# Performance work log

Measured on AMD Instinct MI355X. Metric: run time of the kernel, lower is better.

## Reference

```python
import jax, jax.numpy as jnp
import numpy as np

N = 50000      # total nodes
E = 500000     # edges
D = 128        # in_channels
B = 50         # graphs in batch
NPG = N // B   # nodes per graph (equal-sized graphs)
RATIO = 0.5
ALPHA = 0.6


def setup_inputs() -> dict:
    key = jax.random.key(0)
    ks = jax.random.split(key, 8)
    x = jax.random.normal(ks[0], (N, D), dtype=jnp.float32)
    edge_index = jax.random.randint(ks[1], (2, E), 0, N, dtype=jnp.int32)
    batch = jnp.repeat(jnp.arange(B, dtype=jnp.int32), NPG)  # sorted, equal blocks
    s = 1.0 / np.sqrt(D)
    # GCNConv(D,1) for structure score
    W_s = jax.random.normal(ks[2], (D, 1), dtype=jnp.float32) * s
    b_s = jnp.zeros((1,), dtype=jnp.float32)
    # Linear(D,1) for feature score
    W_f = jax.random.normal(ks[3], (1, D), dtype=jnp.float32) * s
    b_f = jnp.zeros((1,), dtype=jnp.float32)
    # GCNConv(D,D) fusion layer
    W_fu = jax.random.normal(ks[4], (D, D), dtype=jnp.float32) * s
    b_fu = jnp.zeros((D,), dtype=jnp.float32)
    return {"x": x, "edge_index": edge_index, "batch": batch,
            "W_s": W_s, "b_s": b_s, "W_f": W_f, "b_f": b_f,
            "W_fu": W_fu, "b_fu": b_fu}


def gcn_conv(x, src, dst, W, b, n):
    """PyG GCNConv: add self loops, symmetric D^-1/2 (A+I) D^-1/2 @ (xW) + b."""
    xw = x @ W                                  # [n, out]
    loop = jnp.arange(n, dtype=src.dtype)
    s = jnp.concatenate([src, loop])
    d = jnp.concatenate([dst, loop])
    deg = jax.ops.segment_sum(jnp.ones_like(s, dtype=xw.dtype), d, num_segments=n)
    dinv = jax.lax.rsqrt(jnp.maximum(deg, 1e-12))
    norm = dinv[s] * dinv[d]                    # [E+n]
    out = jax.ops.segment_sum(norm[:, None] * xw[s], d, num_segments=n)
    return out + b


def reference(x, edge_index, batch, W_s, b_s, W_f, b_f, W_fu, b_fu):
    src, dst = edge_index[0], edge_index[1]
    # fused score: alpha * structure (GCN) + (1-alpha) * feature (Linear)
    score_s = gcn_conv(x, src, dst, W_s, b_s, N)[:, 0]          # [N]
    score_f = (x @ W_f.T + b_f)[:, 0]                           # [N]
    score = jnp.tanh(ALPHA * score_s + (1.0 - ALPHA) * score_f)
    # per-graph top-k (equal-sized graphs -> dense [B, NPG] view, like the torch topk)
    k = int(np.ceil(RATIO * NPG))
    dense = score.reshape(B, NPG)
    order = jnp.argsort(-dense, axis=-1)                        # descending
    offsets = (jnp.arange(B, dtype=jnp.int32) * NPG)[:, None]
    perm = (order[:, :k].astype(jnp.int32) + offsets).reshape(-1)  # [B*k]
    # fusion conv on full graph, then gather selected nodes
    x_fused = gcn_conv(x, src, dst, W_fu, b_fu, N)              # [N, D]
    x_ae = x_fused[perm]                                        # [B*k, D]
    x_out = x_ae * score[perm][:, None]                         # multiplier == 1
    batch_out = batch[perm]
    # filter_adj: remap node ids, keep edges with both endpoints selected
    nodemap = jnp.full((N,), -1, dtype=jnp.int32).at[perm].set(
        jnp.arange(perm.shape[0], dtype=jnp.int32))
    r, c = nodemap[src], nodemap[dst]
    m = (r >= 0) & (c >= 0)
    edge_index_new = jnp.stack([r[m], c[m]], axis=0)
    return (x_out, edge_index_new, batch_out, perm, x_ae)
```

## Files before the change

### kernel.cpp

```cpp
#include <hip/hip_runtime.h>
#include <math.h>

#define N_NODES 50000
#define N_EDGES 500000
#define DIM     128
#define NGRAPH  50
#define NPGC    1000
#define KSEL    500
#define SORT_N  1024
#define NBE     489
#define NBN     49
#define GEMM_BLKS 391
#define DEG_BLKS  1954
#define DOTS_BLKS 12500
#define NDINV     196
#define GATH_BLKS 6250


__global__ __launch_bounds__(256) void k1_gemm_deg(const float* __restrict__ x,
                                                   const float* __restrict__ W,
                                                   float* __restrict__ xw,
                                                   const int* __restrict__ dst,
                                                   int* __restrict__ deg) {
    __shared__ float lds[16384];
    int t = threadIdx.x;
    if (blockIdx.x >= GEMM_BLKS) {
        int e = (blockIdx.x - GEMM_BLKS) * 256 + t;
        if (e < N_EDGES) atomicAdd(&deg[dst[e]], 1);
        return;
    }
    float* Wt = lds;
    float* Xt = lds + 64 * DIM;
    int cg = t & 15;
    int ng = t >> 4;
    int node_base = blockIdx.x * 128;

    float4 acc[8][2];
    #pragma unroll
    for (int nn = 0; nn < 8; nn++) {
        acc[nn][0] = make_float4(0.f, 0.f, 0.f, 0.f);
        acc[nn][1] = make_float4(0.f, 0.f, 0.f, 0.f);
    }
    for (int half = 0; half < 2; half++) {
        const float4* Wg = (const float4*)(W + half * 64 * DIM);
        float4* Wl = (float4*)Wt;
        #pragma unroll
        for (int i = 0; i < 8; i++) {
            int f = t + i * 256;
            Wl[f] = Wg[f];
        }
        #pragma unroll
        for (int i = 0; i < 8; i++) {
            int f = t + i * 256;
            int row = f >> 4, col = f & 15;
            int node = node_base + row;
            float4 v = make_float4(0.f, 0.f, 0.f, 0.f);
            if (node < N_NODES) v = *(const float4*)&x[(size_t)node * DIM + half * 64 + col * 4];
            *(float4*)&Xt[(row << 6) + ((col ^ (row & 15)) << 2)] = v;
        }
        __syncthreads();
        #pragma unroll 2
        for (int kc = 0; kc < 16; kc++) {
            int k = kc << 2;
            float4 wa[4], wb[4];
            #pragma unroll
            for (int kk = 0; kk < 4; kk++) {
                wa[kk] = *(const float4*)&Wt[(k + kk) * DIM + (cg << 2)];
                wb[kk] = *(const float4*)&Wt[(k + kk) * DIM + (cg << 2) + 64];
            }
            int csw = (kc ^ ng) << 2;
            #pragma unroll
            for (int nn = 0; nn < 8; nn++) {
                float4 xv = *(const float4*)&Xt[((ng + (nn << 4)) << 6) + csw];
                acc[nn][0].x += xv.x * wa[0].x + xv.y * wa[1].x + xv.z * wa[2].x + xv.w * wa[3].x;
                acc[nn][0].y += xv.x * wa[0].y + xv.y * wa[1].y + xv.z * wa[2].y + xv.w * wa[3].y;
                acc[nn][0].z += xv.x * wa[0].z + xv.y * wa[1].z + xv.z * wa[2].z + xv.w * wa[3].z;
                acc[nn][0].w += xv.x * wa[0].w + xv.y * wa[1].w + xv.z * wa[2].w + xv.w * wa[3].w;
                acc[nn][1].x += xv.x * wb[0].x + xv.y * wb[1].x + xv.z * wb[2].x + xv.w * wb[3].x;
                acc[nn][1].y += xv.x * wb[0].y + xv.y * wb[1].y + xv.z * wb[2].y + xv.w * wb[3].y;
                acc[nn][1].z += xv.x * wb[0].z + xv.y * wb[1].z + xv.z * wb[2].z + xv.w * wb[3].z;
                acc[nn][1].w += xv.x * wb[0].w + xv.y * wb[1].w + xv.z * wb[2].w + xv.w * wb[3].w;
            }
        }
        __syncthreads();
    }
    #pragma unroll
    for (int nn = 0; nn < 8; nn++) {
        int node = node_base + ng + (nn << 4);
        if (node < N_NODES) {
            *(float4*)&xw[(size_t)node * DIM + (cg << 2)]      = acc[nn][0];
            *(float4*)&xw[(size_t)node * DIM + (cg << 2) + 64] = acc[nn][1];
        }
    }
}


__global__ __launch_bounds__(256) void k2_dots_scan_dinv(const int* __restrict__ deg,
                                                         int* __restrict__ rowoff,
                                                         int* __restrict__ bsumsN,
                                                         const float* __restrict__ x,
                                                         const float* __restrict__ Ws,
                                                         const float* __restrict__ Wf,
                                                         const float* __restrict__ bf,
                                                         double* __restrict__ pack,
                                                         float* __restrict__ dinvf,
                                                         double* __restrict__ sf) {
    int t = threadIdx.x;
    int lane = t & 63, wid = t >> 6;
    int bid = blockIdx.x;
    if (bid < DOTS_BLKS) {
        int node = bid * 4 + wid;
        const float* xr = x + (size_t)node * DIM;
        double x1 = (double)xr[lane], x2 = (double)xr[lane + 64];
        double ps = x1 * (double)Ws[lane] + x2 * (double)Ws[lane + 64];
        double pf = x1 * (double)Wf[lane] + x2 * (double)Wf[lane + 64];
        for (int off = 32; off > 0; off >>= 1) {
            ps += __shfl_down(ps, off, 64);
            pf += __shfl_down(pf, off, 64);
        }
        if (lane == 0) {
            pack[2 * node + 1] = ps;
            sf[node] = pf + (double)bf[0];
        }
        return;
    }
    if (bid < DOTS_BLKS + NBN) {
        __shared__ int ws4[4];
        int base = (bid - DOTS_BLKS) * 1024 + t * 4;
        int v0 = (base + 0 < N_NODES) ? deg[base + 0] : 0;
        int v1 = (base + 1 < N_NODES) ? deg[base + 1] : 0;
        int v2 = (base + 2 < N_NODES) ? deg[base + 2] : 0;
        int v3 = (base + 3 < N_NODES) ? deg[base + 3] : 0;
        int s4 = v0 + v1 + v2 + v3;
        int incl = s4;
        #pragma unroll
        for (int off = 1; off < 64; off <<= 1) {
            int u = __shfl_up(incl, off, 64);
            if (lane >= off) incl += u;
        }
        if (lane == 63) ws4[wid] = incl;
        __syncthreads();
        int woff = 0;
        #pragma unroll
        for (int w = 0; w < 4; w++) if (w < wid) woff += ws4[w];
        int excl = incl - s4 + woff;
        if (base + 0 < N_NODES) rowoff[base + 0] = excl;
        if (base + 1 < N_NODES) rowoff[base + 1] = excl + v0;
        if (base + 2 < N_NODES) rowoff[base + 2] = excl + v0 + v1;
        if (base + 3 < N_NODES) rowoff[base + 3] = excl + v0 + v1 + v2;
        if (t == 255) bsumsN[bid - DOTS_BLKS] = woff + incl;
        return;
    }
    int i = (bid - DOTS_BLKS - NBN) * 256 + t;
    if (i < N_NODES) {
        double di = 1.0 / sqrt((double)(deg[i] + 1));
        pack[2 * i] = di;
        dinvf[i] = (float)di;
    }
}


__global__ __launch_bounds__(256) void k3_csr(const int* __restrict__ src,
                                              const int* __restrict__ dst,
                                              const int* __restrict__ rowoff,
                                              const int* __restrict__ bsumsN,
                                              int* __restrict__ cursor,
                                              int* __restrict__ csr) {
    __shared__ int bsN[64];
    int t = threadIdx.x;
    if (t < 64) {
        int v = (t < NBN) ? bsumsN[t] : 0;
        int incl = v;
        #pragma unroll
        for (int off = 1; off < 64; off <<= 1) {
            int u = __shfl_up(incl, off, 64);
            if (t >= off) incl += u;
        }
        bsN[t] = incl - v;
    }
    __syncthreads();
    int e = blockIdx.x * 256 + t;
    if (e >= N_EDGES) return;
    int d = dst[e];
    int pos = rowoff[d] + bsN[d >> 10] + atomicAdd(&cursor[d], 1);
    csr[pos] = src[e];
}


__global__ __launch_bounds__(256) void k3b_score(const int* __restrict__ csr,
                                                 const int* __restrict__ rowoff,
                                                 const int* __restrict__ bsumsN,
                                                 const int* __restrict__ deg,
                                                 const double* __restrict__ pack,
                                                 double* __restrict__ score_sd) {
    __shared__ int bsN[64];
    int t = threadIdx.x;
    if (t < 64) {
        int v = (t < NBN) ? bsumsN[t] : 0;
        int incl = v;
        #pragma unroll
        for (int off = 1; off < 64; off <<= 1) {
            int u = __shfl_up(incl, off, 64);
            if (t >= off) incl += u;
        }
        bsN[t] = incl - v;
    }
    __syncthreads();
    int node = blockIdx.x * 256 + t;
    if (node >= N_NODES) return;
    int base = rowoff[node] + bsN[node >> 10];
    int cnt  = deg[node];
    double acc0 = 0.0, acc1 = 0.0;
    int i = 0;
    for (; i + 2 <= cnt; i += 2) {
        int s0 = csr[base + i];
        int s1 = csr[base + i + 1];
        double2 p0 = ((const double2*)pack)[s0];
        double2 p1 = ((const double2*)pack)[s1];
        acc0 += p0.x * p0.y;
        acc1 += p1.x * p1.y;
    }
    if (i < cnt) {
        int s0 = csr[base + i];
        double2 p0 = ((const double2*)pack)[s0];
        acc0 += p0.x * p0.y;
    }
    score_sd[node] = pack[2 * node] * (acc0 + acc1);
}


__global__ __launch_bounds__(512) void k4_topk(const double* __restrict__ score_sd,
                                               const double* __restrict__ pack,
                                               const double* __restrict__ sf,
                                               const float* __restrict__ bs,
                                               const int* __restrict__ batch,
                                               int* __restrict__ perm, int* __restrict__ nodemap,
                                               float* __restrict__ scoref_sel,
                                               float* __restrict__ out, long o2, long o3) {
    __shared__ double key[SORT_N];
    __shared__ int    idx[SORT_N];
    int g = blockIdx.x, t = threadIdx.x;
    const double A = 0.6, OMA = 1.0 - 0.6;
    double bsv = (double)bs[0];
    for (int i = t; i < SORT_N; i += 512) {
        if (i < NPGC) {
            int node = g * NPGC + i;
            double2 p = ((const double2*)pack)[node];
            double tot = score_sd[node] + p.x * p.x * p.y + bsv;
            key[i] = tanh(A * tot + OMA * sf[node]);
            idx[i] = i;
        } else { key[i] = -1e300; idx[i] = i; }
    }
    __syncthreads();
    for (int size = 2; size <= SORT_N; size <<= 1) {
        for (int stride = size >> 1; stride > 0; stride >>= 1) {
            int a = ((t & ~(stride - 1)) << 1) | (t & (stride - 1));
            int b = a | stride;
            bool descFirst = ((a & size) == 0);
            double ka = key[a], kb = key[b];
            int ia = idx[a], ib = idx[b];
            bool aAfterB = (ka < kb) || (ka == kb && ia > ib);
            if (descFirst ? aAfterB : !aAfterB) {
                key[a] = kb; key[b] = ka;
                idx[a] = ib; idx[b] = ia;
            }
            __syncthreads();
        }
    }
    for (int j = t; j < KSEL; j += 512) {
        int node = g * NPGC + idx[j];
        int pos  = g * KSEL + j;
        perm[pos]        = node;
        nodemap[node]    = pos + 1;
        scoref_sel[pos]  = (float)key[j];
        out[o2 + pos]    = (float)batch[node];
        out[o3 + pos]    = (float)node;
    }
}


__global__ __launch_bounds__(256) void k5_escan_gather(const int* __restrict__ src,
                                                       const int* __restrict__ dst,
                                                       const int* __restrict__ nodemap,
                                                       int* __restrict__ epos,
                                                       int* __restrict__ bsumsE,
                                                       const float* __restrict__ xw,
                                                       const int* __restrict__ perm,
                                                       const int* __restrict__ rowoff,
                                                       const int* __restrict__ bsumsN,
                                                       const int* __restrict__ deg,
                                                       const int* __restrict__ csr,
                                                       const float* __restrict__ dinvf,
                                                       const float* __restrict__ scoref_sel,
                                                       const float* __restrict__ b_fu,
                                                       float* __restrict__ out, long o4) {
    int t = threadIdx.x;
    int lane = t & 63, wid = t >> 6;
    if (blockIdx.x < NBE) {
        __shared__ int ws4[4];
        int base = blockIdx.x * 1024 + t * 4;
        int v0 = 0, v1 = 0, v2 = 0, v3 = 0;
        if (base + 0 < N_EDGES) v0 = (nodemap[src[base + 0]] > 0 && nodemap[dst[base + 0]] > 0);
        if (base + 1 < N_EDGES) v1 = (nodemap[src[base + 1]] > 0 && nodemap[dst[base + 1]] > 0);
        if (base + 2 < N_EDGES) v2 = (nodemap[src[base + 2]] > 0 && nodemap[dst[base + 2]] > 0);
        if (base + 3 < N_EDGES) v3 = (nodemap[src[base + 3]] > 0 && nodemap[dst[base + 3]] > 0);
        int s4 = v0 + v1 + v2 + v3;
        int incl = s4;
        #pragma unroll
        for (int off = 1; off < 64; off <<= 1) {
            int u = __shfl_up(incl, off, 64);
            if (lane >= off) incl += u;
        }
        if (lane == 63) ws4[wid] = incl;
        __syncthreads();
        int woff = 0;
        #pragma unroll
        for (int w = 0; w < 4; w++) if (w < wid) woff += ws4[w];
        int excl = incl - s4 + woff;
        if (base + 0 < N_EDGES) epos[base + 0] = excl;
        if (base + 1 < N_EDGES) epos[base + 1] = excl + v0;
        if (base + 2 < N_EDGES) epos[base + 2] = excl + v0 + v1;
        if (base + 3 < N_EDGES) epos[base + 3] = excl + v0 + v1 + v2;
        if (t == 255) bsumsE[blockIdx.x] = woff + incl;
        return;
    }
    __shared__ int bsN[64];
    if (t < 64) {
        int v = (t < NBN) ? bsumsN[t] : 0;
        int incl = v;
        #pragma unroll
        for (int off = 1; off < 64; off <<= 1) {
            int u = __shfl_up(incl, off, 64);
            if (t >= off) incl += u;
        }
        bsN[t] = incl - v;
    }
    __syncthreads();
    int wave = (blockIdx.x - NBE) * 4 + wid;
    int p = perm[wave];
    float dpf = dinvf[p];
    int c2 = lane * 2;
    float2 v = ((const float2*)(xw + (size_t)p * DIM))[lane];
    float nself = dpf * dpf;
    float ax = nself * v.x, ay = nself * v.y;
    int beg = rowoff[p] + bsN[p >> 10], cnt = deg[p];
    int i = 0;
    for (; i + 2 <= cnt; i += 2) {
        int s0 = csr[beg + i];
        int s1 = csr[beg + i + 1];
        float2 u0 = ((const float2*)(xw + (size_t)s0 * DIM))[lane];
        float2 u1 = ((const float2*)(xw + (size_t)s1 * DIM))[lane];
        float n0 = dinvf[s0] * dpf, n1 = dinvf[s1] * dpf;
        ax += n0 * u0.x; ay += n0 * u0.y;
        ax += n1 * u1.x; ay += n1 * u1.y;
    }
    if (i < cnt) {
        int s0 = csr[beg + i];
        float2 u0 = ((const float2*)(xw + (size_t)s0 * DIM))[lane];
        float n0 = dinvf[s0] * dpf;
        ax += n0 * u0.x; ay += n0 * u0.y;
    }
    ax += b_fu[c2];
    ay += b_fu[c2 + 1];
    float sc = scoref_sel[wave];
    size_t ro = (size_t)wave * DIM + c2;
    out[o4 + ro]     = ax;
    out[o4 + ro + 1] = ay;
    out[ro]          = ax * sc;
    out[ro + 1]      = ay * sc;
}


__global__ __launch_bounds__(256) void k6_compact(const int* __restrict__ src,
                                                  const int* __restrict__ dst,
                                                  const int* __restrict__ nodemap,
                                                  const int* __restrict__ epos,
                                                  const int* __restrict__ bsumsE,
                                                  float* __restrict__ out_edges, long M) {
    __shared__ int bsE[512];
    int t = threadIdx.x;
    if (t < 64) {
        int carry = 0;
        #pragma unroll
        for (int c = 0; c < 8; c++) {
            int i = c * 64 + t;
            int v = (i < NBE) ? bsumsE[i] : 0;
            int incl = v;
            #pragma unroll
            for (int off = 1; off < 64; off <<= 1) {
                int u = __shfl_up(incl, off, 64);
                if (t >= off) incl += u;
            }
            if (i < 512) bsE[i] = incl - v + carry;
            carry += __shfl(incl, 63, 64);
        }
    }
    __syncthreads();
    int e = blockIdx.x * 256 + t;
    if (e >= N_EDGES) return;
    int r = nodemap[src[e]], c = nodemap[dst[e]];
    if (r > 0 && c > 0) {
        int pos = epos[e] + bsE[e >> 10];
        out_edges[pos]     = (float)(r - 1);
        out_edges[M + pos] = (float)(c - 1);
    }
}


extern "C" void kernel_launch(void* const* d_in, const int* in_sizes, int n_in,
                              void* d_out, int out_size, void* d_ws, size_t ws_size,
                              hipStream_t stream) {
    const float* x    = (const float*)d_in[0];
    const int*   ei   = (const int*)d_in[1];
    const int*   src  = ei;
    const int*   dst  = ei + N_EDGES;
    const int*   batch= (const int*)d_in[2];
    const float* W_s  = (const float*)d_in[3];
    const float* b_s  = (const float*)d_in[4];
    const float* W_f  = (const float*)d_in[5];
    const float* b_f  = (const float*)d_in[6];
    const float* W_fu = (const float*)d_in[7];
    const float* b_fu = (const float*)d_in[8];
    float* out = (float*)d_out;

    char* wsp = (char*)d_ws;
    size_t off = 0;
    auto take = [&](size_t bytes) -> char* {
        char* p = wsp + off;
        off = (off + bytes + 255) & ~(size_t)255;
        return p;
    };
    char*   zbase      = wsp;
    int*    deg        = (int*)   take((size_t)N_NODES * 4);
    int*    cursor     = (int*)   take((size_t)N_NODES * 4);
    int*    nodemap    = (int*)   take((size_t)N_NODES * 4);
    size_t  zbytes     = off;
    double* score_sd   = (double*)take((size_t)N_NODES * 8);
    double* pack       = (double*)take((size_t)N_NODES * 16);
    double* sf         = (double*)take((size_t)N_NODES * 8);
    float*  dinvf      = (float*) take((size_t)N_NODES * 4);
    float*  scoref_sel = (float*) take((size_t)NGRAPH * KSEL * 4);
    int*    perm       = (int*)   take((size_t)NGRAPH * KSEL * 4);
    int*    rowoff     = (int*)   take((size_t)N_NODES * 4);
    int*    epos       = (int*)   take((size_t)N_EDGES * 4);
    int*    bsumsE     = (int*)   take((size_t)1024 * 4);
    int*    bsumsN     = (int*)   take((size_t)1024 * 4);
    int*    csr        = (int*)   take((size_t)N_EDGES * 4);
    float*  xw         = (float*) take((size_t)N_NODES * DIM * 4);

    long M  = ((long)out_size - 6450000L) / 2;
    long o1 = 3200000L;
    long o2 = o1 + 2 * M;
    long o3 = o2 + (long)NGRAPH * KSEL;
    long o4 = o3 + (long)NGRAPH * KSEL;

    hipMemsetAsync(zbase, 0, zbytes, stream);

    k1_gemm_deg<<<GEMM_BLKS + DEG_BLKS, 256, 0, stream>>>(x, W_fu, xw, dst, deg);
    k2_dots_scan_dinv<<<DOTS_BLKS + NBN + NDINV, 256, 0, stream>>>(deg, rowoff, bsumsN,
                                                                   x, W_s, W_f, b_f,
                                                                   pack, dinvf, sf);
    k3_csr<<<DEG_BLKS, 256, 0, stream>>>(src, dst, rowoff, bsumsN, cursor, csr);
    k3b_score<<<NDINV, 256, 0, stream>>>(csr, rowoff, bsumsN, deg, pack, score_sd);
    k4_topk<<<NGRAPH, 512, 0, stream>>>(score_sd, pack, sf, b_s, batch,
                                        perm, nodemap, scoref_sel, out, o2, o3);
    k5_escan_gather<<<NBE + GATH_BLKS, 256, 0, stream>>>(src, dst, nodemap, epos, bsumsE,
                                                         xw, perm, rowoff, bsumsN, deg, csr,
                                                         dinvf, scoref_sel, b_fu, out, o4);
    k6_compact<<<DEG_BLKS, 256, 0, stream>>>(src, dst, nodemap, epos, bsumsE, out + o1, M);
}
```

Before: 228.3 us.

## Fuse score aggregation into top-k kernel and prefetch GEMM second half

Merges the per-node structure-score aggregation kernel into the per-graph top-k kernel, which now runs with 1024 threads so each thread computes one node's score directly into shared memory. This removes a launch and the score_sd round-trip through global memory. The GEMM kernel now loads the second K-half of W and x into registers while the first half is computed, overlapping global loads with math at the cost of higher register pressure. The batch input is replaced by the graph index, which relies on batch being sorted into equal-sized blocks.

```diff
diff --git a/kernel.cpp b/kernel.cpp
--- a/kernel.cpp
+++ b/kernel.cpp
@@ -41,48 +41,100 @@
         acc[nn][0] = make_float4(0.f, 0.f, 0.f, 0.f);
         acc[nn][1] = make_float4(0.f, 0.f, 0.f, 0.f);
     }
-    for (int half = 0; half < 2; half++) {
-        const float4* Wg = (const float4*)(W + half * 64 * DIM);
+
+    int xrow  = t >> 4, xcol = t & 15;
+    float4 w0[8], x0[8];
+    {
+        const float4* Wg = (const float4*)W;
+        #pragma unroll
+        for (int i = 0; i < 8; i++) w0[i] = Wg[t + i * 256];
+        #pragma unroll
+        for (int i = 0; i < 8; i++) {
+            int node = node_base + xrow + i * 16;
+            x0[i] = make_float4(0.f, 0.f, 0.f, 0.f);
+            if (node < N_NODES) x0[i] = *(const float4*)&x[(size_t)node * DIM + xcol * 4];
+        }
+    }
+    {
         float4* Wl = (float4*)Wt;
         #pragma unroll
+        for (int i = 0; i < 8; i++) Wl[t + i * 256] = w0[i];
+        #pragma unroll
         for (int i = 0; i < 8; i++) {
-            int f = t + i * 256;
-            Wl[f] = Wg[f];
-        }
+            int row = xrow + i * 16;
+            *(float4*)&Xt[(row << 6) + ((xcol ^ (row & 15)) << 2)] = x0[i];
+        }
+    }
+    __syncthreads();
+    float4 w1[8], x1[8];
+    {
+        const float4* Wg = (const float4*)(W + 64 * DIM);
+        #pragma unroll
+        for (int i = 0; i < 8; i++) w1[i] = Wg[t + i * 256];
         #pragma unroll
         for (int i = 0; i < 8; i++) {
-            int f = t + i * 256;
-            int row = f >> 4, col = f & 15;
-            int node = node_base + row;
-            float4 v = make_float4(0.f, 0.f, 0.f, 0.f);
-            if (node < N_NODES) v = *(const float4*)&x[(size_t)node * DIM + half * 64 + col * 4];
-            *(float4*)&Xt[(row << 6) + ((col ^ (row & 15)) << 2)] = v;
-        }
-        __syncthreads();
-        #pragma unroll 2
-        for (int kc = 0; kc < 16; kc++) {
-            int k = kc << 2;
-            float4 wa[4], wb[4];
-            #pragma unroll
-            for (int kk = 0; kk < 4; kk++) {
-                wa[kk] = *(const float4*)&Wt[(k + kk) * DIM + (cg << 2)];
-                wb[kk] = *(const float4*)&Wt[(k + kk) * DIM + (cg << 2) + 64];
-            }
-            int csw = (kc ^ ng) << 2;
-            #pragma unroll
-            for (int nn = 0; nn < 8; nn++) {
-                float4 xv = *(const float4*)&Xt[((ng + (nn << 4)) << 6) + csw];
-                acc[nn][0].x += xv.x * wa[0].x + xv.y * wa[1].x + xv.z * wa[2].x + xv.w * wa[3].x;
-                acc[nn][0].y += xv.x * wa[0].y + xv.y * wa[1].y + xv.z * wa[2].y + xv.w * wa[3].y;
-                acc[nn][0].z += xv.x * wa[0].z + xv.y * wa[1].z + xv.z * wa[2].z + xv.w * wa[3].z;
-                acc[nn][0].w += xv.x * wa[0].w + xv.y * wa[1].w + xv.z * wa[2].w + xv.w * wa[3].w;
-                acc[nn][1].x += xv.x * wb[0].x + xv.y * wb[1].x + xv.z * wb[2].x + xv.w * wb[3].x;
-                acc[nn][1].y += xv.x * wb[0].y + xv.y * wb[1].y + xv.z * wb[2].y + xv.w * wb[3].y;
-                acc[nn][1].z += xv.x * wb[0].z + xv.y * wb[1].z + xv.z * wb[2].z + xv.w * wb[3].z;
-                acc[nn][1].w += xv.x * wb[0].w + xv.y * wb[1].w + xv.z * wb[2].w + xv.w * wb[3].w;
-            }
-        }
-        __syncthreads();
+            int node = node_base + xrow + i * 16;
+            x1[i] = make_float4(0.f, 0.f, 0.f, 0.f);
+            if (node < N_NODES) x1[i] = *(const float4*)&x[(size_t)node * DIM + 64 + xcol * 4];
+        }
+    }
+    #pragma unroll 2
+    for (int kc = 0; kc < 16; kc++) {
+        int k = kc << 2;
+        float4 wa[4], wb[4];
+        #pragma unroll
+        for (int kk = 0; kk < 4; kk++) {
+            wa[kk] = *(const float4*)&Wt[(k + kk) * DIM + (cg << 2)];
+            wb[kk] = *(const float4*)&Wt[(k + kk) * DIM + (cg << 2) + 64];
+        }
+        int csw = (kc ^ ng) << 2;
+        #pragma unroll
+        for (int nn = 0; nn < 8; nn++) {
+            float4 xv = *(const float4*)&Xt[((ng + (nn << 4)) << 6) + csw];
+            acc[nn][0].x += xv.x * wa[0].x + xv.y * wa[1].x + xv.z * wa[2].x + xv.w * wa[3].x;
+            acc[nn][0].y += xv.x * wa[0].y + xv.y * wa[1].y + xv.z * wa[2].y + xv.w * wa[3].y;
+            acc[nn][0].z += xv.x * wa[0].z + xv.y * wa[1].z + xv.z * wa[2].z + xv.w * wa[3].z;
+            acc[nn][0].w += xv.x * wa[0].w + xv.y * wa[1].w + xv.z * wa[2].w + xv.w * wa[3].w;
+            acc[nn][1].x += xv.x * wb[0].x + xv.y * wb[1].x + xv.z * wb[2].x + xv.w * wb[3].x;
+            acc[nn][1].y += xv.x * wb[0].y + xv.y * wb[1].y + xv.z * wb[2].y + xv.w * wb[3].y;
+            acc[nn][1].z += xv.x * wb[0].z + xv.y * wb[1].z + xv.z * wb[2].z + xv.w * wb[3].z;
+            acc[nn][1].w += xv.x * wb[0].w + xv.y * wb[1].w + xv.z * wb[2].w + xv.w * wb[3].w;
+        }
+    }
+    __syncthreads();
+    {
+        float4* Wl = (float4*)Wt;
+        #pragma unroll
+        for (int i = 0; i < 8; i++) Wl[t + i * 256] = w1[i];
+        #pragma unroll
+        for (int i = 0; i < 8; i++) {
+            int row = xrow + i * 16;
+            *(float4*)&Xt[(row << 6) + ((xcol ^ (row & 15)) << 2)] = x1[i];
+        }
+    }
+    __syncthreads();
+    #pragma unroll 2
+    for (int kc = 0; kc < 16; kc++) {
+        int k = kc << 2;
+        float4 wa[4], wb[4];
+        #pragma unroll
+        for (int kk = 0; kk < 4; kk++) {
+            wa[kk] = *(const float4*)&Wt[(k + kk) * DIM + (cg << 2)];
+            wb[kk] = *(const float4*)&Wt[(k + kk) * DIM + (cg << 2) + 64];
+        }
+        int csw = (kc ^ ng) << 2;
+        #pragma unroll
+        for (int nn = 0; nn < 8; nn++) {
+            float4 xv = *(const float4*)&Xt[((ng + (nn << 4)) << 6) + csw];
+            acc[nn][0].x += xv.x * wa[0].x + xv.y * wa[1].x + xv.z * wa[2].x + xv.w * wa[3].x;
+            acc[nn][0].y += xv.x * wa[0].y + xv.y * wa[1].y + xv.z * wa[2].y + xv.w * wa[3].y;
+            acc[nn][0].z += xv.x * wa[0].z + xv.y * wa[1].z + xv.z * wa[2].z + xv.w * wa[3].z;
+            acc[nn][0].w += xv.x * wa[0].w + xv.y * wa[1].w + xv.z * wa[2].w + xv.w * wa[3].w;
+            acc[nn][1].x += xv.x * wb[0].x + xv.y * wb[1].x + xv.z * wb[2].x + xv.w * wb[3].x;
+            acc[nn][1].y += xv.x * wb[0].y + xv.y * wb[1].y + xv.z * wb[2].y + xv.w * wb[3].y;
+            acc[nn][1].z += xv.x * wb[0].z + xv.y * wb[1].z + xv.z * wb[2].z + xv.w * wb[3].z;
+            acc[nn][1].w += xv.x * wb[0].w + xv.y * wb[1].w + xv.z * wb[2].w + xv.w * wb[3].w;
+        }
     }
     #pragma unroll
     for (int nn = 0; nn < 8; nn++) {
@@ -187,14 +239,20 @@
 }
 
 
-__global__ __launch_bounds__(256) void k3b_score(const int* __restrict__ csr,
-                                                 const int* __restrict__ rowoff,
-                                                 const int* __restrict__ bsumsN,
-                                                 const int* __restrict__ deg,
-                                                 const double* __restrict__ pack,
-                                                 double* __restrict__ score_sd) {
-    __shared__ int bsN[64];
-    int t = threadIdx.x;
+__global__ __launch_bounds__(1024) void k4_topk(const int* __restrict__ csr,
+                                                const int* __restrict__ rowoff,
+                                                const int* __restrict__ bsumsN,
+                                                const int* __restrict__ deg,
+                                                const double* __restrict__ pack,
+                                                const double* __restrict__ sf,
+                                                const float* __restrict__ bs,
+                                                int* __restrict__ perm, int* __restrict__ nodemap,
+                                                float* __restrict__ scoref_sel,
+                                                float* __restrict__ out, long o2, long o3) {
+    __shared__ double key[SORT_N];
+    __shared__ int    idx[SORT_N];
+    __shared__ int    bsN[64];
+    int g = blockIdx.x, t = threadIdx.x;
     if (t < 64) {
         int v = (t < NBN) ? bsumsN[t] : 0;
         int incl = v;
@@ -206,74 +264,61 @@
         bsN[t] = incl - v;
     }
     __syncthreads();
-    int node = blockIdx.x * 256 + t;
-    if (node >= N_NODES) return;
-    int base = rowoff[node] + bsN[node >> 10];
-    int cnt  = deg[node];
-    double acc0 = 0.0, acc1 = 0.0;
-    int i = 0;
-    for (; i + 2 <= cnt; i += 2) {
-        int s0 = csr[base + i];
-        int s1 = csr[base + i + 1];
-        double2 p0 = ((const double2*)pack)[s0];
-        double2 p1 = ((const double2*)pack)[s1];
-        acc0 += p0.x * p0.y;
-        acc1 += p1.x * p1.y;
-    }
-    if (i < cnt) {
-        int s0 = csr[base + i];
-        double2 p0 = ((const double2*)pack)[s0];
-        acc0 += p0.x * p0.y;
-    }
-    score_sd[node] = pack[2 * node] * (acc0 + acc1);
-}
-
-
-__global__ __launch_bounds__(512) void k4_topk(const double* __restrict__ score_sd,
-                                               const double* __restrict__ pack,
-                                               const double* __restrict__ sf,
-                                               const float* __restrict__ bs,
-                                               const int* __restrict__ batch,
-                                               int* __restrict__ perm, int* __restrict__ nodemap,
-                                               float* __restrict__ scoref_sel,
-                                               float* __restrict__ out, long o2, long o3) {
-    __shared__ double key[SORT_N];
-    __shared__ int    idx[SORT_N];
-    int g = blockIdx.x, t = threadIdx.x;
     const double A = 0.6, OMA = 1.0 - 0.6;
     double bsv = (double)bs[0];
-    for (int i = t; i < SORT_N; i += 512) {
+    {
+        int i = t;
         if (i < NPGC) {
             int node = g * NPGC + i;
-            double2 p = ((const double2*)pack)[node];
-            double tot = score_sd[node] + p.x * p.x * p.y + bsv;
+            int base = rowoff[node] + bsN[node >> 10];
+            int cnt  = deg[node];
+            double acc0 = 0.0, acc1 = 0.0;
+            int e = 0;
+            for (; e + 2 <= cnt; e += 2) {
+                int s0 = csr[base + e];
+                int s1 = csr[base + e + 1];
+                double2 p0 = ((const double2*)pack)[s0];
+                double2 p1 = ((const double2*)pack)[s1];
+                acc0 += p0.x * p0.y;
+                acc1 += p1.x * p1.y;
+            }
+            if (e < cnt) {
+                int s0 = csr[base + e];
+                double2 p0 = ((const double2*)pack)[s0];
+                acc0 += p0.x * p0.y;
+            }
+            double2 pn = ((const double2*)pack)[node];
+            double tot = pn.x * (acc0 + acc1) + pn.x * pn.x * pn.y + bsv;
             key[i] = tanh(A * tot + OMA * sf[node]);
             idx[i] = i;
-        } else { key[i] = -1e300; idx[i] = i; }
+        } else if (i < SORT_N) { key[i] = -1e300; idx[i] = i; }
     }
     __syncthreads();
     for (int size = 2; size <= SORT_N; size <<= 1) {
         for (int stride = size >> 1; stride > 0; stride >>= 1) {
-            int a = ((t & ~(stride - 1)) << 1) | (t & (stride - 1));
-            int b = a | stride;
-            bool descFirst = ((a & size) == 0);
-            double ka = key[a], kb = key[b];
-            int ia = idx[a], ib = idx[b];
-            bool aAfterB = (ka < kb) || (ka == kb && ia > ib);
-            if (descFirst ? aAfterB : !aAfterB) {
-                key[a] = kb; key[b] = ka;
-                idx[a] = ib; idx[b] = ia;
+            if (t < 512) {
+                int a = ((t & ~(stride - 1)) << 1) | (t & (stride - 1));
+                int b = a | stride;
+                bool descFirst = ((a & size) == 0);
+                double ka = key[a], kb = key[b];
+                int ia = idx[a], ib = idx[b];
+                bool aAfterB = (ka < kb) || (ka == kb && ia > ib);
+                if (descFirst ? aAfterB : !aAfterB) {
+                    key[a] = kb; key[b] = ka;
+                    idx[a] = ib; idx[b] = ia;
+                }
             }
             __syncthreads();
         }
     }
-    for (int j = t; j < KSEL; j += 512) {
+    if (t < KSEL) {
+        int j = t;
         int node = g * NPGC + idx[j];
         int pos  = g * KSEL + j;
         perm[pos]        = node;
         nodemap[node]    = pos + 1;
         scoref_sel[pos]  = (float)key[j];
-        out[o2 + pos]    = (float)batch[node];
+        out[o2 + pos]    = (float)g;
         out[o3 + pos]    = (float)node;
     }
 }
@@ -414,7 +459,6 @@
     const int*   ei   = (const int*)d_in[1];
     const int*   src  = ei;
     const int*   dst  = ei + N_EDGES;
-    const int*   batch= (const int*)d_in[2];
     const float* W_s  = (const float*)d_in[3];
     const float* b_s  = (const float*)d_in[4];
     const float* W_f  = (const float*)d_in[5];
@@ -435,7 +479,6 @@
     int*    cursor     = (int*)   take((size_t)N_NODES * 4);
     int*    nodemap    = (int*)   take((size_t)N_NODES * 4);
     size_t  zbytes     = off;
-    double* score_sd   = (double*)take((size_t)N_NODES * 8);
     double* pack       = (double*)take((size_t)N_NODES * 16);
     double* sf         = (double*)take((size_t)N_NODES * 8);
     float*  dinvf      = (float*) take((size_t)N_NODES * 4);
@@ -461,9 +504,8 @@
                                                                    x, W_s, W_f, b_f,
                                                                    pack, dinvf, sf);
     k3_csr<<<DEG_BLKS, 256, 0, stream>>>(src, dst, rowoff, bsumsN, cursor, csr);
-    k3b_score<<<NDINV, 256, 0, stream>>>(csr, rowoff, bsumsN, deg, pack, score_sd);
-    k4_topk<<<NGRAPH, 512, 0, stream>>>(score_sd, pack, sf, b_s, batch,
-                                        perm, nodemap, scoref_sel, out, o2, o3);
+    k4_topk<<<NGRAPH, 1024, 0, stream>>>(csr, rowoff, bsumsN, deg, pack, sf, b_s,
+                                         perm, nodemap, scoref_sel, out, o2, o3);
     k5_escan_gather<<<NBE + GATH_BLKS, 256, 0, stream>>>(src, dst, nodemap, epos, bsumsE,
                                                          xw, perm, rowoff, bsumsN, deg, csr,
                                                          dinvf, scoref_sel, b_fu, out, o4);
```

Result: slower. 248.5 us (+8.9%).

## Fuse structure-score aggregation into top-k kernel and halve GEMM tile rows

Applied to the files above, without the earlier changes.

The per-node CSR gather that computes the structure score now runs inside the top-k kernel, which uses 1024 threads so each thread handles one node of its graph. This removes one launch and the score_sd round trip through global memory. Separately, the GEMM tile shrinks from 128 to 64 nodes per block, doubling the block count to spread work over more CUs and lowering LDS and register use. The batch output is written as the graph index instead of being read from the batch array. The fused gather runs on only 50 blocks, so its latency may be exposed where the old kernel spread it across 196 blocks.

```diff
diff --git a/kernel.cpp b/kernel.cpp
--- a/kernel.cpp
+++ b/kernel.cpp
@@ -10,7 +10,7 @@
 #define SORT_N  1024
 #define NBE     489
 #define NBN     49
-#define GEMM_BLKS 391
+#define GEMM_BLKS 782
 #define DEG_BLKS  1954
 #define DOTS_BLKS 12500
 #define NDINV     196
@@ -22,7 +22,7 @@
                                                    float* __restrict__ xw,
                                                    const int* __restrict__ dst,
                                                    int* __restrict__ deg) {
-    __shared__ float lds[16384];
+    __shared__ float lds[12288];
     int t = threadIdx.x;
     if (blockIdx.x >= GEMM_BLKS) {
         int e = (blockIdx.x - GEMM_BLKS) * 256 + t;
@@ -33,11 +33,11 @@
     float* Xt = lds + 64 * DIM;
     int cg = t & 15;
     int ng = t >> 4;
-    int node_base = blockIdx.x * 128;
-
-    float4 acc[8][2];
+    int node_base = blockIdx.x * 64;
+
+    float4 acc[4][2];
     #pragma unroll
-    for (int nn = 0; nn < 8; nn++) {
+    for (int nn = 0; nn < 4; nn++) {
         acc[nn][0] = make_float4(0.f, 0.f, 0.f, 0.f);
         acc[nn][1] = make_float4(0.f, 0.f, 0.f, 0.f);
     }
@@ -50,7 +50,7 @@
             Wl[f] = Wg[f];
         }
         #pragma unroll
-        for (int i = 0; i < 8; i++) {
+        for (int i = 0; i < 4; i++) {
             int f = t + i * 256;
             int row = f >> 4, col = f & 15;
             int node = node_base + row;
@@ -70,7 +70,7 @@
             }
             int csw = (kc ^ ng) << 2;
             #pragma unroll
-            for (int nn = 0; nn < 8; nn++) {
+            for (int nn = 0; nn < 4; nn++) {
                 float4 xv = *(const float4*)&Xt[((ng + (nn << 4)) << 6) + csw];
                 acc[nn][0].x += xv.x * wa[0].x + xv.y * wa[1].x + xv.z * wa[2].x + xv.w * wa[3].x;
                 acc[nn][0].y += xv.x * wa[0].y + xv.y * wa[1].y + xv.z * wa[2].y + xv.w * wa[3].y;
@@ -85,7 +85,7 @@
         __syncthreads();
     }
     #pragma unroll
-    for (int nn = 0; nn < 8; nn++) {
+    for (int nn = 0; nn < 4; nn++) {
         int node = node_base + ng + (nn << 4);
         if (node < N_NODES) {
             *(float4*)&xw[(size_t)node * DIM + (cg << 2)]      = acc[nn][0];
@@ -187,14 +187,20 @@
 }
 
 
-__global__ __launch_bounds__(256) void k3b_score(const int* __restrict__ csr,
-                                                 const int* __restrict__ rowoff,
-                                                 const int* __restrict__ bsumsN,
-                                                 const int* __restrict__ deg,
-                                                 const double* __restrict__ pack,
-                                                 double* __restrict__ score_sd) {
-    __shared__ int bsN[64];
-    int t = threadIdx.x;
+__global__ __launch_bounds__(1024) void k4_topk(const int* __restrict__ csr,
+                                                const int* __restrict__ rowoff,
+                                                const int* __restrict__ bsumsN,
+                                                const int* __restrict__ deg,
+                                                const double* __restrict__ pack,
+                                                const double* __restrict__ sf,
+                                                const float* __restrict__ bs,
+                                                int* __restrict__ perm, int* __restrict__ nodemap,
+                                                float* __restrict__ scoref_sel,
+                                                float* __restrict__ out, long o2, long o3) {
+    __shared__ double key[SORT_N];
+    __shared__ int    idx[SORT_N];
+    __shared__ int    bsN[64];
+    int g = blockIdx.x, t = threadIdx.x;
     if (t < 64) {
         int v = (t < NBN) ? bsumsN[t] : 0;
         int incl = v;
@@ -206,74 +212,61 @@
         bsN[t] = incl - v;
     }
     __syncthreads();
-    int node = blockIdx.x * 256 + t;
-    if (node >= N_NODES) return;
-    int base = rowoff[node] + bsN[node >> 10];
-    int cnt  = deg[node];
-    double acc0 = 0.0, acc1 = 0.0;
-    int i = 0;
-    for (; i + 2 <= cnt; i += 2) {
-        int s0 = csr[base + i];
-        int s1 = csr[base + i + 1];
-        double2 p0 = ((const double2*)pack)[s0];
-        double2 p1 = ((const double2*)pack)[s1];
-        acc0 += p0.x * p0.y;
-        acc1 += p1.x * p1.y;
-    }
-    if (i < cnt) {
-        int s0 = csr[base + i];
-        double2 p0 = ((const double2*)pack)[s0];
-        acc0 += p0.x * p0.y;
-    }
-    score_sd[node] = pack[2 * node] * (acc0 + acc1);
-}
-
-
-__global__ __launch_bounds__(512) void k4_topk(const double* __restrict__ score_sd,
-                                               const double* __restrict__ pack,
-                                               const double* __restrict__ sf,
-                                               const float* __restrict__ bs,
-                                               const int* __restrict__ batch,
-                                               int* __restrict__ perm, int* __restrict__ nodemap,
-                                               float* __restrict__ scoref_sel,
-                                               float* __restrict__ out, long o2, long o3) {
-    __shared__ double key[SORT_N];
-    __shared__ int    idx[SORT_N];
-    int g = blockIdx.x, t = threadIdx.x;
     const double A = 0.6, OMA = 1.0 - 0.6;
     double bsv = (double)bs[0];
-    for (int i = t; i < SORT_N; i += 512) {
+    {
+        int i = t;
         if (i < NPGC) {
             int node = g * NPGC + i;
-            double2 p = ((const double2*)pack)[node];
-            double tot = score_sd[node] + p.x * p.x * p.y + bsv;
+            int base = rowoff[node] + bsN[node >> 10];
+            int cnt  = deg[node];
+            double acc0 = 0.0, acc1 = 0.0;
+            int e = 0;
+            for (; e + 2 <= cnt; e += 2) {
+                int s0 = csr[base + e];
+                int s1 = csr[base + e + 1];
+                double2 p0 = ((const double2*)pack)[s0];
+                double2 p1 = ((const double2*)pack)[s1];
+                acc0 += p0.x * p0.y;
+                acc1 += p1.x * p1.y;
+            }
+            if (e < cnt) {
+                int s0 = csr[base + e];
+                double2 p0 = ((const double2*)pack)[s0];
+                acc0 += p0.x * p0.y;
+            }
+            double2 pn = ((const double2*)pack)[node];
+            double tot = pn.x * (acc0 + acc1) + pn.x * pn.x * pn.y + bsv;
             key[i] = tanh(A * tot + OMA * sf[node]);
             idx[i] = i;
-        } else { key[i] = -1e300; idx[i] = i; }
+        } else if (i < SORT_N) { key[i] = -1e300; idx[i] = i; }
     }
     __syncthreads();
     for (int size = 2; size <= SORT_N; size <<= 1) {
         for (int stride = size >> 1; stride > 0; stride >>= 1) {
-            int a = ((t & ~(stride - 1)) << 1) | (t & (stride - 1));
-            int b = a | stride;
-            bool descFirst = ((a & size) == 0);
-            double ka = key[a], kb = key[b];
-            int ia = idx[a], ib = idx[b];
-            bool aAfterB = (ka < kb) || (ka == kb && ia > ib);
-            if (descFirst ? aAfterB : !aAfterB) {
-                key[a] = kb; key[b] = ka;
-                idx[a] = ib; idx[b] = ia;
+            if (t < 512) {
+                int a = ((t & ~(stride - 1)) << 1) | (t & (stride - 1));
+                int b = a | stride;
+                bool descFirst = ((a & size) == 0);
+                double ka = key[a], kb = key[b];
+                int ia = idx[a], ib = idx[b];
+                bool aAfterB = (ka < kb) || (ka == kb && ia > ib);
+                if (descFirst ? aAfterB : !aAfterB) {
+                    key[a] = kb; key[b] = ka;
+                    idx[a] = ib; idx[b] = ia;
+                }
             }
             __syncthreads();
         }
     }
-    for (int j = t; j < KSEL; j += 512) {
+    if (t < KSEL) {
+        int j = t;
         int node = g * NPGC + idx[j];
         int pos  = g * KSEL + j;
         perm[pos]        = node;
         nodemap[node]    = pos + 1;
         scoref_sel[pos]  = (float)key[j];
-        out[o2 + pos]    = (float)batch[node];
+        out[o2 + pos]    = (float)g;
         out[o3 + pos]    = (float)node;
     }
 }
@@ -414,7 +407,6 @@
     const int*   ei   = (const int*)d_in[1];
     const int*   src  = ei;
     const int*   dst  = ei + N_EDGES;
-    const int*   batch= (const int*)d_in[2];
     const float* W_s  = (const float*)d_in[3];
     const float* b_s  = (const float*)d_in[4];
     const float* W_f  = (const float*)d_in[5];
@@ -435,7 +427,6 @@
     int*    cursor     = (int*)   take((size_t)N_NODES * 4);
     int*    nodemap    = (int*)   take((size_t)N_NODES * 4);
     size_t  zbytes     = off;
-    double* score_sd   = (double*)take((size_t)N_NODES * 8);
     double* pack       = (double*)take((size_t)N_NODES * 16);
     double* sf         = (double*)take((size_t)N_NODES * 8);
     float*  dinvf      = (float*) take((size_t)N_NODES * 4);
@@ -461,9 +452,8 @@
                                                                    x, W_s, W_f, b_f,
                                                                    pack, dinvf, sf);
     k3_csr<<<DEG_BLKS, 256, 0, stream>>>(src, dst, rowoff, bsumsN, cursor, csr);
-    k3b_score<<<NDINV, 256, 0, stream>>>(csr, rowoff, bsumsN, deg, pack, score_sd);
-    k4_topk<<<NGRAPH, 512, 0, stream>>>(score_sd, pack, sf, b_s, batch,
-                                        perm, nodemap, scoref_sel, out, o2, o3);
+    k4_topk<<<NGRAPH, 1024, 0, stream>>>(csr, rowoff, bsumsN, deg, pack, sf, b_s,
+                                         perm, nodemap, scoref_sel, out, o2, o3);
     k5_escan_gather<<<NBE + GATH_BLKS, 256, 0, stream>>>(src, dst, nodemap, epos, bsumsE,
                                                          xw, perm, rowoff, bsumsN, deg, csr,
                                                          dinvf, scoref_sel, b_fu, out, o4);
```

After: 240.2 us. 1.05x slower.
